# Performance work log

Hardware: AMD Instinct MI355X
Metric: run time of the kernel (lower is better)

## Reference

```python
import jax, jax.numpy as jnp
import numpy as np

SEQ_LEN = 131072
NUM_NODES = 256
NUM_CAUSES = 16
NUM_FEATURES = 100
NUM_OUTPUTS = 1
NOISE_STD = 0.01


def _build_dag_mask(N, C, p, rng):
    # upper-triangular random adjacency; roots (0..C-1) have no parents;
    # every non-root gets at least one parent (mirrors _build_random_dag)
    A = (rng.random((N, N)) < p) & np.triu(np.ones((N, N), bool), k=1)
    A[:, :C] = False
    for j in range(C, N):
        if not A[:j, j].any():
            A[rng.integers(0, j), j] = True
    return A.astype(np.int32)


def setup_inputs() -> dict:
    key = jax.random.key(0)
    k1, k2, k3 = jax.random.split(key, 3)
    rng = np.random.default_rng(0)
    S, N, C = SEQ_LEN, NUM_NODES, NUM_CAUSES
    causes = jax.random.normal(k1, (S, C), dtype=jnp.float32)
    W = jax.random.normal(k2, (N, N), dtype=jnp.float32)  # edge weights w_ij ~ N(0,1)
    eps = jax.random.normal(k3, (S, N - C), dtype=jnp.float32)  # unit noise, scaled by NOISE_STD
    mask = jnp.asarray(_build_dag_mask(N, C, 0.3, rng))
    act_id = jnp.asarray(rng.integers(0, 4, size=(N - C,)), dtype=jnp.int32)
    # y from a sink-like last node; X from sorted sample of remaining non-root nodes
    y_idx = jnp.asarray([N - 1], dtype=jnp.int64)
    X_idx = jnp.asarray(np.sort(rng.choice(np.arange(C, N - 1), size=NUM_FEATURES, replace=False)), dtype=jnp.int64)
    return {"causes": causes, "W": W, "eps": eps, "mask": mask, "act_id": act_id, "X_idx": X_idx, "y_idx": y_idx}


def reference(causes, W, eps, mask, act_id, X_idx, y_idx):
    S, C = causes.shape
    N = W.shape[0]
    Wm = W * mask.astype(W.dtype)                      # [N,N] masked edge weights (parent i -> node j)
    vals0 = jnp.zeros((S, N), W.dtype).at[:, :C].set(causes)
    Wcols = Wm.T[C:]                                   # [N-C, N] incoming-weight rows per non-root node
    eps_t = eps.T                                      # [N-C, S]
    branches = [lambda z: z, jnp.tanh, jax.nn.relu, jax.nn.sigmoid]

    def step(carry, xs):
        vals, idx = carry
        w_col, e, a = xs
        z = vals @ w_col + jnp.float32(NOISE_STD) * e  # weighted parent sum + noise, [S]
        v = jax.lax.switch(a, branches, z)
        vals = vals.at[:, idx].set(v)
        return (vals, idx + 1), None

    (vals, _), _ = jax.lax.scan(step, (vals0, jnp.int32(C)), (Wcols, eps_t, act_id))
    X = vals[:, X_idx]                                 # [S, num_features]
    y = vals[:, y_idx]                                 # [S, 1]
    bad = jnp.isnan(X).any() | jnp.isnan(y).any()
    X = jnp.where(bad, jnp.float32(0.0), X)
    y = jnp.where(bad, jnp.float32(-100.0), y)
    return X, y[:, 0]                                  # num_outputs == 1 -> squeeze
```

## Files before the change

kernel.cpp:

```cpp
#include <hip/hip_runtime.h>
#include <hip/hip_bf16.h>
#include <hip/hip_fp16.h>


typedef _Float16 half8 __attribute__((ext_vector_type(8)));
typedef float    f32x4 __attribute__((ext_vector_type(4)));

constexpr int S_LEN    = 131072;
constexpr int N_NODES  = 256;
constexpr int N_CAUSES = 16;
constexpr int N_COMP   = 240;
constexpr int N_FEAT   = 100;
constexpr float NOISE  = 0.01f;
constexpr float VSC    = 0.0625f;
constexpr float VSCI   = 16.0f;

constexpr int KE_tab[16]  = {0,32,64,64,96,96,128,128,160,160,192,192,224,224,256,256};
constexpr int OFF_tab[16] = {0,0,1024,3072,5120,8192,11264,15360,19456,24576,29696,
                             35840,41984,49152,56320,64512};

__constant__ int c_KE[16]  = {0,32,64,64,96,96,128,128,160,160,192,192,224,224,256,256};
__constant__ int c_OFF[16] = {0,0,1024,3072,5120,8192,11264,15360,19456,24576,29696,
                              35840,41984,49152,56320,64512};

__device__ _Float16 g_WT[72704];
__device__ float    g_Wtri[15 * 256];

__device__ __forceinline__ bool sniff_binary64(const void* p) {
    const unsigned* u = (const unsigned*)p;
    bool ok = true;
    for (int i = 0; i < 64; ++i) ok = ok && (u[i] <= 1u);
    return ok;
}
__device__ __forceinline__ bool sniff_is_bf16(const void* p) {
    const unsigned* u = (const unsigned*)p;
    bool ok = true;
    for (int i = 0; i < 16; ++i) {
        unsigned e = ((u[i] << 16) >> 23) & 0xffu;
        ok = ok && (e >= 100u) && (e <= 132u);
    }
    return ok;
}
__device__ __forceinline__ float bflo(unsigned u) { return __uint_as_float(u << 16); }
__device__ __forceinline__ float bfhi(unsigned u) { return __uint_as_float(u & 0xffff0000u); }

__device__ __forceinline__ void load16(const void* base, long long off, bool isbf, float* o) {
    if (isbf) {
        const uint4* p = (const uint4*)((const unsigned short*)base + off);
        uint4 a = p[0], b = p[1];
        o[0]=bflo(a.x); o[1]=bfhi(a.x); o[2]=bflo(a.y); o[3]=bfhi(a.y);
        o[4]=bflo(a.z); o[5]=bfhi(a.z); o[6]=bflo(a.w); o[7]=bfhi(a.w);
        o[8]=bflo(b.x); o[9]=bfhi(b.x); o[10]=bflo(b.y); o[11]=bfhi(b.y);
        o[12]=bflo(b.z); o[13]=bfhi(b.z); o[14]=bflo(b.w); o[15]=bfhi(b.w);
    } else {
        const float4* p = (const float4*)((const float*)base + off);
        float4 x0=p[0], x1=p[1], x2=p[2], x3=p[3];
        o[0]=x0.x; o[1]=x0.y; o[2]=x0.z; o[3]=x0.w;
        o[4]=x1.x; o[5]=x1.y; o[6]=x1.z; o[7]=x1.w;
        o[8]=x2.x; o[9]=x2.y; o[10]=x2.z; o[11]=x2.w;
        o[12]=x3.x; o[13]=x3.y; o[14]=x3.z; o[15]=x3.w;
    }
}

__device__ __forceinline__ float hw_exp2(float x) {
    float r; asm("v_exp_f32 %0, %1" : "=v"(r) : "v"(x)); return r;
}
__device__ __forceinline__ float hw_rcp(float x) {
    float r; asm("v_rcp_f32 %0, %1" : "=v"(r) : "v"(x)); return r;
}
__device__ __forceinline__ float fast_tanh(float x) {
    float t = hw_exp2(x * 2.88539008177792681f);
    return 1.0f - 2.0f * hw_rcp(t + 1.0f);
}
__device__ __forceinline__ float fast_sigmoid(float x) {
    return hw_rcp(1.0f + hw_exp2(x * -1.44269504088896341f));
}

__global__ void prep_kernel(const void* __restrict__ A, const void* __restrict__ B) {
    __shared__ int s_mA, s_wbf;
    if (threadIdx.x == 0) {
        s_mA  = sniff_binary64(A) ? 1 : 0;
        s_wbf = sniff_is_bf16(s_mA ? B : A) ? 1 : 0;
    }
    __syncthreads();
    const int*  maskp = (const int*)(s_mA ? A : B);
    const void* Wp    = s_mA ? B : A;
    const int k = blockIdx.x + 1, j0 = 16 * k, KE = c_KE[k], OFF = c_OFF[k];
    const int tid = threadIdx.x;

    for (int n = 0; n < 16; ++n) {
        const int j = j0 + n;
        for (int kk = tid; kk < KE; kk += 256) {
            const int gi = kk * N_NODES + j;
            float w = 0.0f;
            if (maskp[gi])
                w = s_wbf ? __bfloat162float(((const __hip_bfloat16*)Wp)[gi])
                          : ((const float*)Wp)[gi];
            const _Float16 hi = (_Float16)w;
            const _Float16 lo = (_Float16)(w - (float)hi);
            g_WT[OFF + n * KE + kk]           = hi;
            g_WT[OFF + 16 * KE + n * KE + kk] = lo;
        }
    }
    {
        const int l = tid >> 4, i = tid & 15;
        const int gi = (j0 + l) * N_NODES + (j0 + i);
        float w = 0.0f;
        if (l < i && maskp[gi])
            w = s_wbf ? __bfloat162float(((const __hip_bfloat16*)Wp)[gi])
                      : ((const float*)Wp)[gi];
        g_Wtri[(k - 1) * 256 + tid] = w;
    }
}

#define MFMA16(a, b, c) __builtin_amdgcn_mfma_f32_16x16x32_f16((a), (b), (c), 0, 0, 0)

template<int K>
__device__ __forceinline__ void do_chunk(
    const int lane, const long long sg,
    const void* __restrict__ eps, const bool ebf,
    half8 (&vf)[4][8],
    float* __restrict__ Zbuf, _Float16* __restrict__ stag,
    const short* __restrict__ xpos, const int* __restrict__ act_id,
    float* __restrict__ outX, float* __restrict__ outY, const int yi)
{
    constexpr int j0  = 16 * K;
    constexpr int KE  = KE_tab[K];
    constexpr int NST = KE / 32;
    constexpr int OFF = OFF_tab[K];

    const int mrow = lane & 15;
    const int quad = lane >> 4;

    float ev[16];
    load16(eps, sg * (long long)N_COMP + (j0 - N_CAUSES), ebf, ev);

    const _Float16* __restrict__ bp = g_WT + OFF + mrow * KE + (quad << 3);

    f32x4 acc0 = {0.f,0.f,0.f,0.f}, acc1 = {0.f,0.f,0.f,0.f};
    f32x4 acc2 = {0.f,0.f,0.f,0.f}, acc3 = {0.f,0.f,0.f,0.f};

    #pragma unroll
    for (int t = 0; t < NST; ++t) {
        const half8 bh = *(const half8*)(bp + (t << 5));
        const half8 bl = *(const half8*)(bp + 16 * KE + (t << 5));
        acc0 = MFMA16(vf[0][t], bh, acc0);
        acc1 = MFMA16(vf[1][t], bh, acc1);
        acc2 = MFMA16(vf[2][t], bh, acc2);
        acc3 = MFMA16(vf[3][t], bh, acc3);
        acc0 = MFMA16(vf[0][t], bl, acc0);
        acc1 = MFMA16(vf[1][t], bl, acc1);
        acc2 = MFMA16(vf[2][t], bl, acc2);
        acc3 = MFMA16(vf[3][t], bl, acc3);
    }

    {
        const int r0 = quad << 2;
        #pragma unroll
        for (int r = 0; r < 4; ++r) {
            Zbuf[(r0 + r)      * 21 + mrow] = acc0[r] * VSCI;
            Zbuf[(16 + r0 + r) * 21 + mrow] = acc1[r] * VSCI;
            Zbuf[(32 + r0 + r) * 21 + mrow] = acc2[r] * VSCI;
            Zbuf[(48 + r0 + r) * 21 + mrow] = acc3[r] * VSCI;
        }
    }
    __builtin_amdgcn_wave_barrier();

    float zz[16];
    #pragma unroll
    for (int i = 0; i < 16; ++i) zz[i] = Zbuf[lane * 21 + i];

    const float* __restrict__ tri = g_Wtri + (K - 1) * 256;
    float vn[16];
    half8 h0, h1;
    #pragma unroll
    for (int i = 0; i < 16; ++i) {
        float z = zz[i] + NOISE * ev[i];
        #pragma unroll
        for (int l = 0; l < i; ++l) z += tri[(l << 4) + i] * vn[l];
        const int a = act_id[j0 - N_CAUSES + i];
        if (a == 1)      z = fast_tanh(z);
        else if (a == 2) z = fmaxf(z, 0.0f);
        else if (a == 3) z = fast_sigmoid(z);
        vn[i] = z;
        if (i < 8) h0[i] = (_Float16)(z * VSC);
        else       h1[i - 8] = (_Float16)(z * VSC);
        const int xp = xpos[j0 - N_CAUSES + i];
        if (xp >= 0) outX[xp] = z;
        if (j0 + i == yi) outY[sg] = z;
    }

    *(half8*)(stag + lane * 24)     = h0;
    *(half8*)(stag + lane * 24 + 8) = h1;
    __builtin_amdgcn_wave_barrier();

    constexpr int TT = K >> 1;
    constexpr int HB = (K & 1) << 1;
    const int hq = lane >> 4;
    if (hq == HB || hq == HB + 1) {
        const int boff = (hq - HB) << 3;
        #pragma unroll
        for (int q = 0; q < 4; ++q)
            vf[q][TT] = *(const half8*)(stag + (q * 16 + (lane & 15)) * 24 + boff);
    }
    __builtin_amdgcn_wave_barrier();
}

__global__ __launch_bounds__(64, 2)
void scm_kernel(const void* __restrict__ causes,
                const void* __restrict__ eps,
                const int* __restrict__ act_id,
                const void* __restrict__ xidx_raw,
                const int* __restrict__ yidx_raw,
                float* __restrict__ out,
                long long ybase) {
    __shared__ __align__(16) float    Zbuf[64 * 21];
    __shared__ __align__(16) _Float16 stag[64 * 24];
    __shared__ short xpos[N_COMP];

    const int lane = threadIdx.x;
    const long long sg = (long long)blockIdx.x * 64 + lane;

    for (int t = lane; t < N_COMP; t += 64) xpos[t] = -1;
    const unsigned long long* x64 = (const unsigned long long*)xidx_raw;
    const int*                x32 = (const int*)xidx_raw;
    const bool is64 = ((x64[0] >> 32) == 0ull);
    __builtin_amdgcn_wave_barrier();
    for (int f = lane; f < N_FEAT; f += 64) {
        const int ix = is64 ? (int)x64[f] : x32[f];
        xpos[ix - N_CAUSES] = (short)f;
    }
    __builtin_amdgcn_wave_barrier();
    const int yi  = yidx_raw[0];
    const bool cbf = sniff_is_bf16(causes);
    const bool ebf = sniff_is_bf16(eps);

    half8 vz;
    #pragma unroll
    for (int e = 0; e < 8; ++e) vz[e] = (_Float16)0.0f;
    half8 vf[4][8];
    #pragma unroll
    for (int q = 0; q < 4; ++q) {
        #pragma unroll
        for (int t = 0; t < 8; ++t) vf[q][t] = vz;
    }

    {
        float cv[16];
        load16(causes, sg * (long long)N_CAUSES, cbf, cv);
        half8 c0, c1;
        #pragma unroll
        for (int i = 0; i < 8; ++i) {
            c0[i] = (_Float16)(cv[i] * VSC);
            c1[i] = (_Float16)(cv[8 + i] * VSC);
        }
        *(half8*)(stag + lane * 24)     = c0;
        *(half8*)(stag + lane * 24 + 8) = c1;
        __builtin_amdgcn_wave_barrier();
        const int hq = lane >> 4;
        if (hq < 2) {
            #pragma unroll
            for (int q = 0; q < 4; ++q)
                vf[q][0] = *(const half8*)(stag + (q * 16 + (lane & 15)) * 24 + (hq << 3));
        }
        __builtin_amdgcn_wave_barrier();
    }

    float* outX = out + sg * N_FEAT;
    float* outY = out + ybase;

    do_chunk< 1>(lane, sg, eps, ebf, vf, Zbuf, stag, xpos, act_id, outX, outY, yi);
    do_chunk< 2>(lane, sg, eps, ebf, vf, Zbuf, stag, xpos, act_id, outX, outY, yi);
    do_chunk< 3>(lane, sg, eps, ebf, vf, Zbuf, stag, xpos, act_id, outX, outY, yi);
    do_chunk< 4>(lane, sg, eps, ebf, vf, Zbuf, stag, xpos, act_id, outX, outY, yi);
    do_chunk< 5>(lane, sg, eps, ebf, vf, Zbuf, stag, xpos, act_id, outX, outY, yi);
    do_chunk< 6>(lane, sg, eps, ebf, vf, Zbuf, stag, xpos, act_id, outX, outY, yi);
    do_chunk< 7>(lane, sg, eps, ebf, vf, Zbuf, stag, xpos, act_id, outX, outY, yi);
    do_chunk< 8>(lane, sg, eps, ebf, vf, Zbuf, stag, xpos, act_id, outX, outY, yi);
    do_chunk< 9>(lane, sg, eps, ebf, vf, Zbuf, stag, xpos, act_id, outX, outY, yi);
    do_chunk<10>(lane, sg, eps, ebf, vf, Zbuf, stag, xpos, act_id, outX, outY, yi);
    do_chunk<11>(lane, sg, eps, ebf, vf, Zbuf, stag, xpos, act_id, outX, outY, yi);
    do_chunk<12>(lane, sg, eps, ebf, vf, Zbuf, stag, xpos, act_id, outX, outY, yi);
    do_chunk<13>(lane, sg, eps, ebf, vf, Zbuf, stag, xpos, act_id, outX, outY, yi);
    do_chunk<14>(lane, sg, eps, ebf, vf, Zbuf, stag, xpos, act_id, outX, outY, yi);
    do_chunk<15>(lane, sg, eps, ebf, vf, Zbuf, stag, xpos, act_id, outX, outY, yi);
}

extern "C" void kernel_launch(void* const* d_in, const int* in_sizes, int n_in,
                              void* d_out, int out_size, void* d_ws, size_t ws_size,
                              hipStream_t stream) {
    int ic = 0, iw = 1, ie = 2, im = 3, ia = 4, ix = 5, iy = 6;
    int c = -1, e = -1, a = -1, x = -1, y = -1, m1 = -1, m2 = -1;
    for (int i = 0; i < n_in; ++i) {
        switch (in_sizes[i]) {
            case S_LEN * N_CAUSES:   c = i; break;
            case S_LEN * N_COMP:     e = i; break;
            case N_COMP:             a = i; break;
            case N_FEAT:             x = i; break;
            case 1:                  y = i; break;
            case N_NODES * N_NODES:  (m1 < 0 ? m1 : m2) = i; break;
        }
    }
    if (c >= 0 && e >= 0 && a >= 0 && x >= 0 && y >= 0 && m1 >= 0 && m2 >= 0) {
        ic = c; ie = e; ia = a; ix = x; iy = y; iw = m1; im = m2;
    }

    const void* causes = d_in[ic];
    const void* TA     = d_in[iw];
    const void* TB     = d_in[im];
    const void* eps    = d_in[ie];
    const int*  act_id = (const int*)d_in[ia];
    const void* xidx   = d_in[ix];
    const int*  yidx   = (const int*)d_in[iy];
    float*      out    = (float*)d_out;
    const long long ybase = (long long)out_size - S_LEN;

    prep_kernel<<<15, 256, 0, stream>>>(TA, TB);
    scm_kernel<<<S_LEN / 64, 64, 0, stream>>>(causes, eps, act_id, xidx, yidx, out, ybase);
}
```

Measured before the change: 408.9 us.

## Stage X outputs feature-major in workspace and transpose with a separate kernel

```diff
diff --git a/kernel.cpp b/kernel.cpp
--- a/kernel.cpp
+++ b/kernel.cpp
@@ -122,6 +122,7 @@
     half8 (&vf)[4][8],
     float* __restrict__ Zbuf, _Float16* __restrict__ stag,
     const short* __restrict__ xpos, const int* __restrict__ act_id,
+    float* __restrict__ wsX,
     float* __restrict__ outX, float* __restrict__ outY, const int yi)
 {
     constexpr int j0  = 16 * K;
@@ -186,7 +187,10 @@
         if (i < 8) h0[i] = (_Float16)(z * VSC);
         else       h1[i - 8] = (_Float16)(z * VSC);
         const int xp = xpos[j0 - N_CAUSES + i];
-        if (xp >= 0) outX[xp] = z;
+        if (xp >= 0) {
+            if (wsX) wsX[(long long)xp * S_LEN + sg] = z;
+            else     outX[xp] = z;
+        }
         if (j0 + i == yi) outY[sg] = z;
     }
 
@@ -213,6 +217,7 @@
                 const void* __restrict__ xidx_raw,
                 const int* __restrict__ yidx_raw,
                 float* __restrict__ out,
+                float* __restrict__ wsX,
                 long long ybase) {
     __shared__ __align__(16) float    Zbuf[64 * 21];
     __shared__ __align__(16) _Float16 stag[64 * 24];
@@ -269,21 +274,43 @@
     float* outX = out + sg * N_FEAT;
     float* outY = out + ybase;
 
-    do_chunk< 1>(lane, sg, eps, ebf, vf, Zbuf, stag, xpos, act_id, outX, outY, yi);
-    do_chunk< 2>(lane, sg, eps, ebf, vf, Zbuf, stag, xpos, act_id, outX, outY, yi);
-    do_chunk< 3>(lane, sg, eps, ebf, vf, Zbuf, stag, xpos, act_id, outX, outY, yi);
-    do_chunk< 4>(lane, sg, eps, ebf, vf, Zbuf, stag, xpos, act_id, outX, outY, yi);
-    do_chunk< 5>(lane, sg, eps, ebf, vf, Zbuf, stag, xpos, act_id, outX, outY, yi);
-    do_chunk< 6>(lane, sg, eps, ebf, vf, Zbuf, stag, xpos, act_id, outX, outY, yi);
-    do_chunk< 7>(lane, sg, eps, ebf, vf, Zbuf, stag, xpos, act_id, outX, outY, yi);
-    do_chunk< 8>(lane, sg, eps, ebf, vf, Zbuf, stag, xpos, act_id, outX, outY, yi);
-    do_chunk< 9>(lane, sg, eps, ebf, vf, Zbuf, stag, xpos, act_id, outX, outY, yi);
-    do_chunk<10>(lane, sg, eps, ebf, vf, Zbuf, stag, xpos, act_id, outX, outY, yi);
-    do_chunk<11>(lane, sg, eps, ebf, vf, Zbuf, stag, xpos, act_id, outX, outY, yi);
-    do_chunk<12>(lane, sg, eps, ebf, vf, Zbuf, stag, xpos, act_id, outX, outY, yi);
-    do_chunk<13>(lane, sg, eps, ebf, vf, Zbuf, stag, xpos, act_id, outX, outY, yi);
-    do_chunk<14>(lane, sg, eps, ebf, vf, Zbuf, stag, xpos, act_id, outX, outY, yi);
-    do_chunk<15>(lane, sg, eps, ebf, vf, Zbuf, stag, xpos, act_id, outX, outY, yi);
+    do_chunk< 1>(lane, sg, eps, ebf, vf, Zbuf, stag, xpos, act_id, wsX, outX, outY, yi);
+    do_chunk< 2>(lane, sg, eps, ebf, vf, Zbuf, stag, xpos, act_id, wsX, outX, outY, yi);
+    do_chunk< 3>(lane, sg, eps, ebf, vf, Zbuf, stag, xpos, act_id, wsX, outX, outY, yi);
+    do_chunk< 4>(lane, sg, eps, ebf, vf, Zbuf, stag, xpos, act_id, wsX, outX, outY, yi);
+    do_chunk< 5>(lane, sg, eps, ebf, vf, Zbuf, stag, xpos, act_id, wsX, outX, outY, yi);
+    do_chunk< 6>(lane, sg, eps, ebf, vf, Zbuf, stag, xpos, act_id, wsX, outX, outY, yi);
+    do_chunk< 7>(lane, sg, eps, ebf, vf, Zbuf, stag, xpos, act_id, wsX, outX, outY, yi);
+    do_chunk< 8>(lane, sg, eps, ebf, vf, Zbuf, stag, xpos, act_id, wsX, outX, outY, yi);
+    do_chunk< 9>(lane, sg, eps, ebf, vf, Zbuf, stag, xpos, act_id, wsX, outX, outY, yi);
+    do_chunk<10>(lane, sg, eps, ebf, vf, Zbuf, stag, xpos, act_id, wsX, outX, outY, yi);
+    do_chunk<11>(lane, sg, eps, ebf, vf, Zbuf, stag, xpos, act_id, wsX, outX, outY, yi);
+    do_chunk<12>(lane, sg, eps, ebf, vf, Zbuf, stag, xpos, act_id, wsX, outX, outY, yi);
+    do_chunk<13>(lane, sg, eps, ebf, vf, Zbuf, stag, xpos, act_id, wsX, outX, outY, yi);
+    do_chunk<14>(lane, sg, eps, ebf, vf, Zbuf, stag, xpos, act_id, wsX, outX, outY, yi);
+    do_chunk<15>(lane, sg, eps, ebf, vf, Zbuf, stag, xpos, act_id, wsX, outX, outY, yi);
+}
+
+__global__ __launch_bounds__(256)
+void xpose_kernel(const float* __restrict__ ws, float* __restrict__ out) {
+    __shared__ float tile[64 * 100];
+    const int tid = threadIdx.x;
+    const long long s0 = (long long)blockIdx.x * 64;
+    const int f = tid >> 6;
+    const int s = tid & 63;
+    #pragma unroll
+    for (int g = 0; g < 25; ++g) {
+        const int ff = f + g * 4;
+        tile[s * 100 + ff] = ws[(long long)ff * S_LEN + s0 + s];
+    }
+    __syncthreads();
+    float4* o4 = (float4*)(out + s0 * N_FEAT);
+    const float4* t4 = (const float4*)tile;
+    #pragma unroll
+    for (int g = 0; g < 7; ++g) {
+        const int idx = g * 256 + tid;
+        if (idx < 1600) o4[idx] = t4[idx];
+    }
 }
 
 extern "C" void kernel_launch(void* const* d_in, const int* in_sizes, int n_in,
@@ -315,6 +342,12 @@
     float*      out    = (float*)d_out;
     const long long ybase = (long long)out_size - S_LEN;
 
+    const bool usews = ws_size >= (size_t)N_FEAT * S_LEN * sizeof(float);
+    float* wsX = usews ? (float*)d_ws : nullptr;
+
     prep_kernel<<<15, 256, 0, stream>>>(TA, TB);
-    scm_kernel<<<S_LEN / 64, 64, 0, stream>>>(causes, eps, act_id, xidx, yidx, out, ybase);
-}
+    scm_kernel<<<S_LEN / 64, 64, 0, stream>>>(causes, eps, act_id, xidx, yidx,
+                                              out, wsX, ybase);
+    if (usews)
+        xpose_kernel<<<S_LEN / 64, 256, 0, stream>>>(wsX, out);
+}
```

After: 356.0 us. -12.9%, faster.
